# Kernel optimization log

Hardware: AMD Instinct MI355X
Metric: run time of the kernel (lower is better)

The kernel has to match this reference:

```python
import jax, jax.numpy as jnp
import numpy as np
import math

D_EMB = 1024
N_HEADS = 16
SCALE = 0.02
B, T = 4, 2048


def _norm(x):
    # torch.std_mean default: unbiased std (ddof=1) over last dim
    m = jnp.mean(x, axis=-1, keepdims=True)
    s = jnp.std(x, axis=-1, keepdims=True, ddof=1)
    return (x - m) / (s + 1e-05)


def setup_inputs() -> dict:
    key = jax.random.key(0)
    kx, kw = jax.random.split(key)
    x = jax.random.normal(kx, (B, D_EMB, T), dtype=jnp.float32)
    qkv = jax.random.normal(kw, (3, N_HEADS, D_EMB, D_EMB // N_HEADS), dtype=jnp.float32) * SCALE
    return {"x": x, "qkv": qkv}


def reference(x, qkv):
    Bsz, D, Tlen = x.shape
    H = qkv.shape[1]
    # (3, B, H, T, d_head)
    h = jnp.einsum('bdt,nhde->nbhte', x, qkv)
    q, k, v = h[0], h[1], h[2]
    q = _norm(q)
    k = _norm(k)
    scale = math.sqrt(D // H)  # torch: sqrt(d_emb // H)
    attn = jnp.einsum('bhte,bhse->bhts', q, k) / scale  # [B,H,T,T]
    attn = jax.nn.softmax(attn, axis=-1)
    out = jnp.einsum('bhts,bhse->bhet', attn, v)  # [B,H,d_head,T]
    return out.reshape(Bsz, D, Tlen)
```

## Files before the change

### kernel.cpp

```cpp
#include <hip/hip_runtime.h>
#include <hip/hip_bf16.h>

#define B_SZ 4
#define NHEADS 16
#define T_SZ 2048
#define DE 1024
#define DH 64
#define BH (B_SZ*NHEADS)
#define SCL 0.18033688011112042f

typedef __attribute__((ext_vector_type(8))) short short8;
typedef __attribute__((ext_vector_type(4))) float float4v;
typedef __attribute__((ext_vector_type(2))) unsigned int uint2v;

__device__ __forceinline__ short f2bf(float f) {
    __hip_bfloat16 h = __float2bfloat16(f);
    return *reinterpret_cast<short*>(&h);
}
__device__ __forceinline__ unsigned int pack_bf2(float a, float b) {
    float2 f; f.x = a; f.y = b;
    __hip_bfloat162 h = __float22bfloat162_rn(f);
    return *reinterpret_cast<unsigned int*>(&h);
}
__device__ __forceinline__ float4v zero4() {
    float4v z = {0.f, 0.f, 0.f, 0.f};
    return z;
}

__global__ __launch_bounds__(256) void transpose_k(const float* __restrict__ src,
                                                   short* __restrict__ dst,
                                                   int R, int C) {
    __shared__ __align__(16) short tile[64 * 65];
    int c0 = blockIdx.x * 64, r0 = blockIdx.y * 64;
    src += (size_t)blockIdx.z * R * C;
    dst += (size_t)blockIdx.z * R * C;
    int tid = threadIdx.x;
#pragma unroll
    for (int it = 0; it < 16; ++it) {
        int idx = it * 256 + tid;
        int rr = idx >> 6, cc = idx & 63;
        tile[cc * 65 + rr] = f2bf(src[(size_t)(r0 + rr) * C + c0 + cc]);
    }
    __syncthreads();
#pragma unroll
    for (int it = 0; it < 16; ++it) {
        int idx = it * 256 + tid;
        int cc = idx >> 6, rr = idx & 63;
        dst[(size_t)(c0 + cc) * R + r0 + rr] = tile[cc * 65 + rr];
    }
}

__global__ __launch_bounds__(256, 2) void qkv_k(const short* __restrict__ XT,
                                                const short* __restrict__ WT,
                                                short* __restrict__ Qw,
                                                short* __restrict__ Kw,
                                                short* __restrict__ Vt) {
    __shared__ __align__(16) short ldsA[256 * 72];
    __shared__ __align__(16) short ldsB[64 * 72];
    int t0 = blockIdx.x * 256;
    int nh = blockIdx.y;
    int b  = blockIdx.z;
    int n = nh >> 4, h = nh & 15;
    int tid = threadIdx.x, wave = tid >> 6, lane = tid & 63;
    int l15 = lane & 15, quad = lane >> 4;

    const short* Arow = XT + ((size_t)b * T_SZ + t0) * DE;
    const short* Brow = WT + (size_t)nh * DH * DE;

    float4v acc[4][4];
#pragma unroll
    for (int mm = 0; mm < 4; ++mm)
#pragma unroll
        for (int j = 0; j < 4; ++j) acc[mm][j] = zero4();

    for (int k0 = 0; k0 < DE; k0 += 64) {
        __syncthreads();
#pragma unroll
        for (int it = 0; it < 8; ++it) {
            int idx = it * 256 + tid;
            int row = idx >> 3, d8 = (idx & 7) * 8;
            *(short8*)&ldsA[row * 72 + d8] =
                *(const short8*)&Arow[(size_t)row * DE + k0 + d8];
        }
#pragma unroll
        for (int it = 0; it < 2; ++it) {
            int idx = it * 256 + tid;
            int row = idx >> 3, d8 = (idx & 7) * 8;
            *(short8*)&ldsB[row * 72 + d8] =
                *(const short8*)&Brow[(size_t)row * DE + k0 + d8];
        }
        __syncthreads();
#pragma unroll
        for (int ks = 0; ks < 2; ++ks) {
            short8 af[4], bf[4];
#pragma unroll
            for (int mm = 0; mm < 4; ++mm)
                af[mm] = *(const short8*)&ldsA[(64 * wave + 16 * mm + l15) * 72 + ks * 32 + quad * 8];
#pragma unroll
            for (int j = 0; j < 4; ++j)
                bf[j] = *(const short8*)&ldsB[(16 * j + l15) * 72 + ks * 32 + quad * 8];
#pragma unroll
            for (int mm = 0; mm < 4; ++mm)
#pragma unroll
                for (int j = 0; j < 4; ++j)
                    acc[mm][j] = __builtin_amdgcn_mfma_f32_16x16x32_bf16(af[mm], bf[j], acc[mm][j], 0, 0, 0);
        }
    }

    int bh = b * NHEADS + h;
#pragma unroll
    for (int mm = 0; mm < 4; ++mm) {
        int tbase = t0 + 64 * wave + 16 * mm;
        if (n < 2) {
            float oscale = (n == 0) ? SCL : 1.0f;
            float mu[4], inv[4];
#pragma unroll
            for (int r = 0; r < 4; ++r) {
                float s1 = 0.f, s2 = 0.f;
#pragma unroll
                for (int j = 0; j < 4; ++j) { float v = acc[mm][j][r]; s1 += v; s2 += v * v; }
                for (int sh = 1; sh < 16; sh <<= 1) {
                    s1 += __shfl_xor(s1, sh, 64);
                    s2 += __shfl_xor(s2, sh, 64);
                }
                mu[r] = s1 * (1.0f / 64.0f);
                float var = (s2 - 64.0f * mu[r] * mu[r]) * (1.0f / 63.0f);
                var = fmaxf(var, 0.0f);
                inv[r] = oscale / (sqrtf(var) + 1e-5f);
            }
            short* dst = (n == 0 ? Qw : Kw) + (size_t)bh * T_SZ * DH;
#pragma unroll
            for (int r = 0; r < 4; ++r) {
                int t = tbase + quad * 4 + r;
#pragma unroll
                for (int j = 0; j < 4; ++j) {
                    float v = (acc[mm][j][r] - mu[r]) * inv[r];
                    dst[(size_t)t * DH + 16 * j + l15] = f2bf(v);
                }
            }
        } else {
#pragma unroll
            for (int r = 0; r < 4; ++r) {
                int t = tbase + quad * 4 + r;
#pragma unroll
                for (int j = 0; j < 4; ++j) {
                    Vt[((size_t)bh * DH + 16 * j + l15) * T_SZ + t] = f2bf(acc[mm][j][r]);
                }
            }
        }
    }
}

__global__ __launch_bounds__(256, 2) void attn_k(const short* __restrict__ Qw,
                                                 const short* __restrict__ Kw,
                                                 const short* __restrict__ Vt,
                                                 float* __restrict__ out) {
    __shared__ __align__(16) char smem[55296];
    short* ldsK = (short*)smem;
    short* ldsV = (short*)(smem + 9216);
    short* ldsP = (short*)(smem + 18432);
    float* ldsO = (float*)smem;

    int t0 = blockIdx.x * 256;
    int bh = blockIdx.y;
    int b = bh >> 4, h = bh & 15;
    int tid = threadIdx.x, wave = tid >> 6, lane = tid & 63;
    int l15 = lane & 15, quad = lane >> 4;
    int tw = t0 + 64 * wave;

    const short* Qp = Qw + (size_t)bh * T_SZ * DH;
    const short* Kp = Kw + (size_t)bh * T_SZ * DH;
    const short* Vp = Vt + (size_t)bh * DH * T_SZ;
    short* Pw = ldsP + wave * 64 * 72;

    short8 qf[4][2];
#pragma unroll
    for (int tt = 0; tt < 4; ++tt)
#pragma unroll
        for (int ks = 0; ks < 2; ++ks)
            qf[tt][ks] = *(const short8*)&Qp[(size_t)(tw + 16 * tt + l15) * DH + ks * 32 + quad * 8];

    float lsum[4] = {0.f, 0.f, 0.f, 0.f};
    float4v o[4][4];
#pragma unroll
    for (int tt = 0; tt < 4; ++tt)
#pragma unroll
        for (int j = 0; j < 4; ++j) o[tt][j] = zero4();

    for (int s0 = 0; s0 < T_SZ; s0 += 64) {
        __syncthreads();
#pragma unroll
        for (int it = 0; it < 2; ++it) {
            int idx = it * 256 + tid;
            int row = idx >> 3, c8 = (idx & 7) * 8;
            *(short8*)&ldsK[row * 72 + c8] = *(const short8*)&Kp[(size_t)(s0 + row) * DH + c8];
            *(short8*)&ldsV[row * 72 + c8] = *(const short8*)&Vp[(size_t)row * T_SZ + s0 + c8];
        }
        __syncthreads();

#pragma unroll
        for (int j = 0; j < 4; ++j) {
            short8 k0 = *(const short8*)&ldsK[(16 * j + l15) * 72 + quad * 8];
            short8 k1 = *(const short8*)&ldsK[(16 * j + l15) * 72 + 32 + quad * 8];
#pragma unroll
            for (int tt = 0; tt < 4; ++tt) {
                float4v z = zero4();
                z = __builtin_amdgcn_mfma_f32_16x16x32_bf16(k0, qf[tt][0], z, 0, 0, 0);
                z = __builtin_amdgcn_mfma_f32_16x16x32_bf16(k1, qf[tt][1], z, 0, 0, 0);
                float p0 = __builtin_amdgcn_exp2f(z[0]);
                float p1 = __builtin_amdgcn_exp2f(z[1]);
                float p2 = __builtin_amdgcn_exp2f(z[2]);
                float p3 = __builtin_amdgcn_exp2f(z[3]);
                lsum[tt] += (p0 + p1) + (p2 + p3);
                uint2v u = { pack_bf2(p0, p1), pack_bf2(p2, p3) };
                *(uint2v*)&Pw[(16 * tt + l15) * 72 + 16 * j + quad * 4] = u;
            }
        }

        short8 pf[4][2];
#pragma unroll
        for (int tt = 0; tt < 4; ++tt) {
            pf[tt][0] = *(const short8*)&Pw[(16 * tt + l15) * 72 + quad * 8];
            pf[tt][1] = *(const short8*)&Pw[(16 * tt + l15) * 72 + 32 + quad * 8];
        }
#pragma unroll
        for (int j = 0; j < 4; ++j) {
            short8 v0 = *(const short8*)&ldsV[(16 * j + l15) * 72 + quad * 8];
            short8 v1 = *(const short8*)&ldsV[(16 * j + l15) * 72 + 32 + quad * 8];
#pragma unroll
            for (int tt = 0; tt < 4; ++tt) {
                o[tt][j] = __builtin_amdgcn_mfma_f32_16x16x32_bf16(pf[tt][0], v0, o[tt][j], 0, 0, 0);
                o[tt][j] = __builtin_amdgcn_mfma_f32_16x16x32_bf16(pf[tt][1], v1, o[tt][j], 0, 0, 0);
            }
        }
    }

    float4v rinv[4];
#pragma unroll
    for (int tt = 0; tt < 4; ++tt) {
        lsum[tt] += __shfl_xor(lsum[tt], 16, 64);
        lsum[tt] += __shfl_xor(lsum[tt], 32, 64);
#pragma unroll
        for (int r = 0; r < 4; ++r)
            rinv[tt][r] = 1.0f / __shfl(lsum[tt], quad * 4 + r, 16);
    }

#pragma unroll
    for (int ph = 0; ph < 2; ++ph) {
        __syncthreads();
        if ((wave >> 1) == ph) {
            float* Ow = ldsO + (wave & 1) * (64 * 68);
#pragma unroll
            for (int tt = 0; tt < 4; ++tt)
#pragma unroll
                for (int j = 0; j < 4; ++j) {
                    float4v ov = o[tt][j] * rinv[tt];
                    *(float4v*)&Ow[(16 * j + l15) * 68 + 16 * tt + quad * 4] = ov;
                }
        }
        __syncthreads();
#pragma unroll
        for (int it = 0; it < 8; ++it) {
            int idx = it * 256 + tid;
            int reg = idx >> 10;
            int rid = idx & 1023;
            int e = rid >> 4, t4 = (rid & 15) * 4;
            *(float4v*)&out[((size_t)(b * DE + h * DH + e)) * T_SZ + t0 + 128 * ph + 64 * reg + t4] =
                *(const float4v*)&ldsO[reg * (64 * 68) + e * 68 + t4];
        }
    }
}

extern "C" void kernel_launch(void* const* d_in, const int* in_sizes, int n_in,
                              void* d_out, int out_size, void* d_ws, size_t ws_size,
                              hipStream_t stream) {
    const float* x = (const float*)d_in[0];
    const float* w = (const float*)d_in[1];
    float* out = (float*)d_out;
    char* ws = (char*)d_ws;

    const size_t XT_BYTES = (size_t)B_SZ * T_SZ * DE * 2;
    const size_t WT_BYTES = (size_t)3 * NHEADS * DH * DE * 2;
    const size_t QKV_BYTES = (size_t)BH * T_SZ * DH * 2;

    short* XT = (short*)(ws);
    short* WT = (short*)(ws + XT_BYTES);
    short* Qw = (short*)(ws + XT_BYTES + WT_BYTES);
    short* Kw = (short*)(ws + XT_BYTES + WT_BYTES + QKV_BYTES);
    short* Vt = (short*)(ws + XT_BYTES + WT_BYTES + 2 * QKV_BYTES);

    transpose_k<<<dim3(T_SZ / 64, DE / 64, B_SZ), 256, 0, stream>>>(x, XT, DE, T_SZ);
    transpose_k<<<dim3(1, DE / 64, 3 * NHEADS), 256, 0, stream>>>(w, WT, DE, DH);
    qkv_k<<<dim3(T_SZ / 256, 3 * NHEADS, B_SZ), 256, 0, stream>>>(XT, WT, Qw, Kw, Vt);
    attn_k<<<dim3(T_SZ / 256, BH), 256, 0, stream>>>(Qw, Kw, Vt, out);
}
```

Baseline: 257.3 us.

## Enlarge QKV GEMM tile, swizzle LDS, compute softmax row sums via MFMA

The QKV projection kernel now runs 512-thread blocks that each compute a 256x256 output tile covering four heads, so every X tile loaded into LDS is reused across four heads instead of one. A 64-element row layout with an XOR swizzle replaces the padded 72-element rows in both kernels to avoid LDS bank conflicts and to shrink LDS use. In the attention kernel, this lets occupancy rise to three blocks per CU. The softmax denominator is now accumulated with extra MFMAs against a ones vector instead of VALU adds and shuffles, which adds matrix work but frees vector ALU. The larger accumulator tile (4x8 float4 per wave) raises register pressure in the QKV kernel.

```diff
diff --git a/kernel.cpp b/kernel.cpp
--- a/kernel.cpp
+++ b/kernel.cpp
@@ -25,6 +25,9 @@
 __device__ __forceinline__ float4v zero4() {
     float4v z = {0.f, 0.f, 0.f, 0.f};
     return z;
+}
+__device__ __forceinline__ int swz(int row, int g) {
+    return row * 64 + (((g) ^ (row & 7)) << 3);
 }
 
 __global__ __launch_bounds__(256) void transpose_k(const float* __restrict__ src,
@@ -50,115 +53,119 @@
     }
 }
 
-__global__ __launch_bounds__(256, 2) void qkv_k(const short* __restrict__ XT,
+__global__ __launch_bounds__(512, 2) void qkv_k(const short* __restrict__ XT,
                                                 const short* __restrict__ WT,
                                                 short* __restrict__ Qw,
                                                 short* __restrict__ Kw,
                                                 short* __restrict__ Vt) {
-    __shared__ __align__(16) short ldsA[256 * 72];
-    __shared__ __align__(16) short ldsB[64 * 72];
-    int t0 = blockIdx.x * 256;
-    int nh = blockIdx.y;
-    int b  = blockIdx.z;
-    int n = nh >> 4, h = nh & 15;
+    __shared__ __align__(16) short ldsA[256 * 64];
+    __shared__ __align__(16) short ldsB[256 * 64];
+    int b  = blockIdx.x >> 3;
+    int t0 = (blockIdx.x & 7) * 256;
+    int n  = blockIdx.y >> 2;
+    int h0 = (blockIdx.y & 3) * 4;
     int tid = threadIdx.x, wave = tid >> 6, lane = tid & 63;
     int l15 = lane & 15, quad = lane >> 4;
+    int wr = wave >> 1, wc = wave & 1;
 
     const short* Arow = XT + ((size_t)b * T_SZ + t0) * DE;
-    const short* Brow = WT + (size_t)nh * DH * DE;
-
-    float4v acc[4][4];
+    const short* Brow = WT + ((size_t)n * 1024 + h0 * 64) * DE;
+
+    float4v acc[4][8];
 #pragma unroll
     for (int mm = 0; mm < 4; ++mm)
 #pragma unroll
-        for (int j = 0; j < 4; ++j) acc[mm][j] = zero4();
+        for (int j = 0; j < 8; ++j) acc[mm][j] = zero4();
 
     for (int k0 = 0; k0 < DE; k0 += 64) {
         __syncthreads();
 #pragma unroll
-        for (int it = 0; it < 8; ++it) {
-            int idx = it * 256 + tid;
-            int row = idx >> 3, d8 = (idx & 7) * 8;
-            *(short8*)&ldsA[row * 72 + d8] =
-                *(const short8*)&Arow[(size_t)row * DE + k0 + d8];
-        }
-#pragma unroll
-        for (int it = 0; it < 2; ++it) {
-            int idx = it * 256 + tid;
-            int row = idx >> 3, d8 = (idx & 7) * 8;
-            *(short8*)&ldsB[row * 72 + d8] =
-                *(const short8*)&Brow[(size_t)row * DE + k0 + d8];
+        for (int it = 0; it < 4; ++it) {
+            int idx = it * 512 + tid;
+            int row = idx >> 3, g = idx & 7;
+            *(short8*)&ldsA[swz(row, g)] =
+                *(const short8*)&Arow[(size_t)row * DE + k0 + g * 8];
+            *(short8*)&ldsB[swz(row, g)] =
+                *(const short8*)&Brow[(size_t)row * DE + k0 + g * 8];
         }
         __syncthreads();
 #pragma unroll
         for (int ks = 0; ks < 2; ++ks) {
-            short8 af[4], bf[4];
+            short8 af[4], bf[8];
 #pragma unroll
             for (int mm = 0; mm < 4; ++mm)
-                af[mm] = *(const short8*)&ldsA[(64 * wave + 16 * mm + l15) * 72 + ks * 32 + quad * 8];
-#pragma unroll
-            for (int j = 0; j < 4; ++j)
-                bf[j] = *(const short8*)&ldsB[(16 * j + l15) * 72 + ks * 32 + quad * 8];
+                af[mm] = *(const short8*)&ldsA[swz(64 * wr + 16 * mm + l15, 4 * ks + quad)];
+#pragma unroll
+            for (int j = 0; j < 8; ++j)
+                bf[j] = *(const short8*)&ldsB[swz(128 * wc + 16 * j + l15, 4 * ks + quad)];
 #pragma unroll
             for (int mm = 0; mm < 4; ++mm)
 #pragma unroll
-                for (int j = 0; j < 4; ++j)
+                for (int j = 0; j < 8; ++j)
                     acc[mm][j] = __builtin_amdgcn_mfma_f32_16x16x32_bf16(af[mm], bf[j], acc[mm][j], 0, 0, 0);
         }
     }
 
-    int bh = b * NHEADS + h;
 #pragma unroll
     for (int mm = 0; mm < 4; ++mm) {
-        int tbase = t0 + 64 * wave + 16 * mm;
-        if (n < 2) {
-            float oscale = (n == 0) ? SCL : 1.0f;
-            float mu[4], inv[4];
-#pragma unroll
-            for (int r = 0; r < 4; ++r) {
-                float s1 = 0.f, s2 = 0.f;
-#pragma unroll
-                for (int j = 0; j < 4; ++j) { float v = acc[mm][j][r]; s1 += v; s2 += v * v; }
-                for (int sh = 1; sh < 16; sh <<= 1) {
-                    s1 += __shfl_xor(s1, sh, 64);
-                    s2 += __shfl_xor(s2, sh, 64);
+        int tbase = t0 + 64 * wr + 16 * mm;
+#pragma unroll
+        for (int jh = 0; jh < 2; ++jh) {
+            int h = h0 + 2 * wc + jh;
+            int bh = b * NHEADS + h;
+            if (n < 2) {
+                float oscale = (n == 0) ? SCL : 1.0f;
+                float mu[4], inv[4];
+#pragma unroll
+                for (int r = 0; r < 4; ++r) {
+                    float s1 = 0.f, s2 = 0.f;
+#pragma unroll
+                    for (int jj = 0; jj < 4; ++jj) {
+                        float v = acc[mm][4 * jh + jj][r];
+                        s1 += v; s2 += v * v;
+                    }
+                    for (int sh = 1; sh < 16; sh <<= 1) {
+                        s1 += __shfl_xor(s1, sh, 64);
+                        s2 += __shfl_xor(s2, sh, 64);
+                    }
+                    mu[r] = s1 * (1.0f / 64.0f);
+                    float var = (s2 - 64.0f * mu[r] * mu[r]) * (1.0f / 63.0f);
+                    var = fmaxf(var, 0.0f);
+                    inv[r] = oscale / (sqrtf(var) + 1e-5f);
                 }
-                mu[r] = s1 * (1.0f / 64.0f);
-                float var = (s2 - 64.0f * mu[r] * mu[r]) * (1.0f / 63.0f);
-                var = fmaxf(var, 0.0f);
-                inv[r] = oscale / (sqrtf(var) + 1e-5f);
-            }
-            short* dst = (n == 0 ? Qw : Kw) + (size_t)bh * T_SZ * DH;
-#pragma unroll
-            for (int r = 0; r < 4; ++r) {
-                int t = tbase + quad * 4 + r;
-#pragma unroll
-                for (int j = 0; j < 4; ++j) {
-                    float v = (acc[mm][j][r] - mu[r]) * inv[r];
-                    dst[(size_t)t * DH + 16 * j + l15] = f2bf(v);
+                short* dst = (n == 0 ? Qw : Kw) + (size_t)bh * T_SZ * DH;
+#pragma unroll
+                for (int r = 0; r < 4; ++r) {
+                    int t = tbase + quad * 4 + r;
+#pragma unroll
+                    for (int jj = 0; jj < 4; ++jj) {
+                        float v = (acc[mm][4 * jh + jj][r] - mu[r]) * inv[r];
+                        dst[(size_t)t * DH + 16 * jj + l15] = f2bf(v);
+                    }
+                }
+            } else {
+#pragma unroll
+                for (int r = 0; r < 4; ++r) {
+                    int t = tbase + quad * 4 + r;
+#pragma unroll
+                    for (int jj = 0; jj < 4; ++jj) {
+                        Vt[((size_t)bh * DH + 16 * jj + l15) * T_SZ + t] =
+                            f2bf(acc[mm][4 * jh + jj][r]);
+                    }
                 }
             }
-        } else {
-#pragma unroll
-            for (int r = 0; r < 4; ++r) {
-                int t = tbase + quad * 4 + r;
-#pragma unroll
-                for (int j = 0; j < 4; ++j) {
-                    Vt[((size_t)bh * DH + 16 * j + l15) * T_SZ + t] = f2bf(acc[mm][j][r]);
-                }
-            }
-        }
-    }
-}
-
-__global__ __launch_bounds__(256, 2) void attn_k(const short* __restrict__ Qw,
+        }
+    }
+}
+
+__global__ __launch_bounds__(256, 3) void attn_k(const short* __restrict__ Qw,
                                                  const short* __restrict__ Kw,
                                                  const short* __restrict__ Vt,
                                                  float* __restrict__ out) {
-    __shared__ __align__(16) char smem[55296];
+    __shared__ __align__(16) char smem[53248];
     short* ldsK = (short*)smem;
-    short* ldsV = (short*)(smem + 9216);
-    short* ldsP = (short*)(smem + 18432);
+    short* ldsV = (short*)(smem + 8192);
+    short* ldsP = (short*)(smem + 16384);
     float* ldsO = (float*)smem;
 
     int t0 = blockIdx.x * 256;
@@ -180,28 +187,33 @@
         for (int ks = 0; ks < 2; ++ks)
             qf[tt][ks] = *(const short8*)&Qp[(size_t)(tw + 16 * tt + l15) * DH + ks * 32 + quad * 8];
 
-    float lsum[4] = {0.f, 0.f, 0.f, 0.f};
+    const short one_bf = (short)0x3F80;
+    short8 ones = {one_bf, one_bf, one_bf, one_bf, one_bf, one_bf, one_bf, one_bf};
+
     float4v o[4][4];
-#pragma unroll
-    for (int tt = 0; tt < 4; ++tt)
+    float4v ol[4];
+#pragma unroll
+    for (int tt = 0; tt < 4; ++tt) {
+        ol[tt] = zero4();
 #pragma unroll
         for (int j = 0; j < 4; ++j) o[tt][j] = zero4();
+    }
 
     for (int s0 = 0; s0 < T_SZ; s0 += 64) {
         __syncthreads();
 #pragma unroll
         for (int it = 0; it < 2; ++it) {
             int idx = it * 256 + tid;
-            int row = idx >> 3, c8 = (idx & 7) * 8;
-            *(short8*)&ldsK[row * 72 + c8] = *(const short8*)&Kp[(size_t)(s0 + row) * DH + c8];
-            *(short8*)&ldsV[row * 72 + c8] = *(const short8*)&Vp[(size_t)row * T_SZ + s0 + c8];
+            int row = idx >> 3, g = idx & 7;
+            *(short8*)&ldsK[swz(row, g)] = *(const short8*)&Kp[(size_t)(s0 + row) * DH + g * 8];
+            *(short8*)&ldsV[swz(row, g)] = *(const short8*)&Vp[(size_t)row * T_SZ + s0 + g * 8];
         }
         __syncthreads();
 
 #pragma unroll
         for (int j = 0; j < 4; ++j) {
-            short8 k0 = *(const short8*)&ldsK[(16 * j + l15) * 72 + quad * 8];
-            short8 k1 = *(const short8*)&ldsK[(16 * j + l15) * 72 + 32 + quad * 8];
+            short8 k0 = *(const short8*)&ldsK[swz(16 * j + l15, quad)];
+            short8 k1 = *(const short8*)&ldsK[swz(16 * j + l15, 4 + quad)];
 #pragma unroll
             for (int tt = 0; tt < 4; ++tt) {
                 float4v z = zero4();
@@ -211,7 +223,6 @@
                 float p1 = __builtin_amdgcn_exp2f(z[1]);
                 float p2 = __builtin_amdgcn_exp2f(z[2]);
                 float p3 = __builtin_amdgcn_exp2f(z[3]);
-                lsum[tt] += (p0 + p1) + (p2 + p3);
                 uint2v u = { pack_bf2(p0, p1), pack_bf2(p2, p3) };
                 *(uint2v*)&Pw[(16 * tt + l15) * 72 + 16 * j + quad * 4] = u;
             }
@@ -222,11 +233,13 @@
         for (int tt = 0; tt < 4; ++tt) {
             pf[tt][0] = *(const short8*)&Pw[(16 * tt + l15) * 72 + quad * 8];
             pf[tt][1] = *(const short8*)&Pw[(16 * tt + l15) * 72 + 32 + quad * 8];
+            ol[tt] = __builtin_amdgcn_mfma_f32_16x16x32_bf16(pf[tt][0], ones, ol[tt], 0, 0, 0);
+            ol[tt] = __builtin_amdgcn_mfma_f32_16x16x32_bf16(pf[tt][1], ones, ol[tt], 0, 0, 0);
         }
 #pragma unroll
         for (int j = 0; j < 4; ++j) {
-            short8 v0 = *(const short8*)&ldsV[(16 * j + l15) * 72 + quad * 8];
-            short8 v1 = *(const short8*)&ldsV[(16 * j + l15) * 72 + 32 + quad * 8];
+            short8 v0 = *(const short8*)&ldsV[swz(16 * j + l15, quad)];
+            short8 v1 = *(const short8*)&ldsV[swz(16 * j + l15, 4 + quad)];
 #pragma unroll
             for (int tt = 0; tt < 4; ++tt) {
                 o[tt][j] = __builtin_amdgcn_mfma_f32_16x16x32_bf16(pf[tt][0], v0, o[tt][j], 0, 0, 0);
@@ -237,13 +250,10 @@
 
     float4v rinv[4];
 #pragma unroll
-    for (int tt = 0; tt < 4; ++tt) {
-        lsum[tt] += __shfl_xor(lsum[tt], 16, 64);
-        lsum[tt] += __shfl_xor(lsum[tt], 32, 64);
+    for (int tt = 0; tt < 4; ++tt)
 #pragma unroll
         for (int r = 0; r < 4; ++r)
-            rinv[tt][r] = 1.0f / __shfl(lsum[tt], quad * 4 + r, 16);
-    }
+            rinv[tt][r] = 1.0f / ol[tt][r];
 
 #pragma unroll
     for (int ph = 0; ph < 2; ++ph) {
@@ -291,6 +301,6 @@
 
     transpose_k<<<dim3(T_SZ / 64, DE / 64, B_SZ), 256, 0, stream>>>(x, XT, DE, T_SZ);
     transpose_k<<<dim3(1, DE / 64, 3 * NHEADS), 256, 0, stream>>>(w, WT, DE, DH);
-    qkv_k<<<dim3(T_SZ / 256, 3 * NHEADS, B_SZ), 256, 0, stream>>>(XT, WT, Qw, Kw, Vt);
+    qkv_k<<<dim3(32, 12), 512, 0, stream>>>(XT, WT, Qw, Kw, Vt);
     attn_k<<<dim3(T_SZ / 256, BH), 256, 0, stream>>>(Qw, Kw, Vt, out);
 }
```

Result: no change. 261.6 us (+1.7%).
